# Performance work log

Hardware: AMD Instinct MI355X
Metric: run time of the kernel (lower is better)

## Reference

```python
import jax, jax.numpy as jnp
import numpy as np

D_MODEL = 1024
NUM_HEADS = 16
DEPTH = D_MODEL // NUM_HEADS


def setup_inputs() -> dict:
    key = jax.random.key(0)
    ks = jax.random.split(key, 11)
    B, S = 2, 2048
    s = 1.0 / np.sqrt(D_MODEL)
    inp = {
        'query': jax.random.normal(ks[0], (B, S, D_MODEL), jnp.float32),
        'key': jax.random.normal(ks[1], (B, S, D_MODEL), jnp.float32),
        'value': jax.random.normal(ks[2], (B, S, D_MODEL), jnp.float32),
        'Wq': jax.random.normal(ks[3], (D_MODEL, D_MODEL), jnp.float32) * s,
        'bq': jnp.zeros((D_MODEL,), jnp.float32),
        'Wk': jax.random.normal(ks[4], (D_MODEL, D_MODEL), jnp.float32) * s,
        'bk': jnp.zeros((D_MODEL,), jnp.float32),
        'Wv': jax.random.normal(ks[5], (D_MODEL, D_MODEL), jnp.float32) * s,
        'bv': jnp.zeros((D_MODEL,), jnp.float32),
        'Wo': jax.random.normal(ks[6], (D_MODEL, D_MODEL), jnp.float32) * s,
        'bo': jnp.zeros((D_MODEL,), jnp.float32),
    }
    return inp


def reference(query, key, value, Wq, bq, Wk, bk, Wv, bv, Wo, bo):
    B, S, _ = query.shape
    # QKV projections (nn.Linear: x @ W.T + b; here W stored as [in,out])
    Q = query @ Wq + bq
    K = key @ Wk + bk
    V = value @ Wv + bv
    # [B, H, S, depth]
    Q = Q.reshape(B, S, NUM_HEADS, DEPTH).transpose(0, 2, 1, 3)
    K = K.reshape(B, S, NUM_HEADS, DEPTH).transpose(0, 2, 1, 3)
    V = V.reshape(B, S, NUM_HEADS, DEPTH).transpose(0, 2, 1, 3)
    scores = jnp.einsum('bhqd,bhkd->bhqk', Q, K) / jnp.sqrt(jnp.float32(DEPTH))
    weights = jax.nn.softmax(scores, axis=-1)
    out = jnp.einsum('bhqk,bhkd->bhqd', weights, V)
    out = out.transpose(0, 2, 1, 3).reshape(B, S, D_MODEL)
    return out @ Wo + bo
```

## Files before the change

### kernel.cpp

```cpp
#include <hip/hip_runtime.h>
#include <stdint.h>

#define D_MODEL 1024
#define NHEAD   16
#define DEPTH   64
#define BATCH   2
#define SEQ     2048
#define M_ROWS  (BATCH*SEQ)

typedef __attribute__((ext_vector_type(8))) short short8;
typedef __attribute__((ext_vector_type(4))) float f32x4;
typedef _Float16 __attribute__((ext_vector_type(8))) half8;
typedef __fp16 __attribute__((ext_vector_type(2))) fp16x2;

__device__ __forceinline__ unsigned short f2b(float f) {
    union { float f; uint32_t u; } v; v.f = f;
    uint32_t r = (v.u + 0x7FFFu + ((v.u >> 16) & 1u)) >> 16;
    return (unsigned short)r;
}
__device__ __forceinline__ unsigned short f2h(float f) {
    union { _Float16 h; unsigned short u; } c; c.h = (_Float16)f; return c.u;
}
__device__ __forceinline__ unsigned int pkh(float a, float b) {
    union { fp16x2 h; unsigned int u; } c;
    c.h = __builtin_amdgcn_cvt_pkrtz(a, b);
    return c.u;
}
__device__ __forceinline__ float exp2fast(float x) {
#if defined(__has_builtin) && __has_builtin(__builtin_amdgcn_exp2f)
    return __builtin_amdgcn_exp2f(x);
#else
    return exp2f(x);
#endif
}

__device__ __forceinline__ void glds16(const void* g, void* l) {
    __builtin_amdgcn_global_load_lds(
        (const __attribute__((address_space(1))) unsigned int*)(uintptr_t)g,
        (__attribute__((address_space(3))) unsigned int*)(unsigned int)(uintptr_t)l,
        16, 0, 0);
}

__global__ __launch_bounds__(256) void prep(
    const float* __restrict__ q, const float* __restrict__ k, const float* __restrict__ v,
    unsigned short* __restrict__ xq, unsigned short* __restrict__ xk, unsigned short* __restrict__ xv,
    const float* __restrict__ w0, const float* __restrict__ w1,
    const float* __restrict__ w2, const float* __restrict__ w3,
    unsigned short* __restrict__ t0, unsigned short* __restrict__ t1,
    unsigned short* __restrict__ t2, unsigned short* __restrict__ t3)
{
    __shared__ unsigned short tile[64][65];
    const int bid = blockIdx.x, tid = threadIdx.x;
    if (bid < 12288) {
        const int t = bid >> 12;
        const float* s = (t == 0) ? q : (t == 1) ? k : v;
        unsigned short* d = (t == 0) ? xq : (t == 1) ? xk : xv;
        int i = (bid & 4095) * 256 + tid;
        float4 val = ((const float4*)s)[i];
        ushort4 u;
        u.x = f2b(val.x); u.y = f2b(val.y); u.z = f2b(val.z); u.w = f2b(val.w);
        ((ushort4*)d)[i] = u;
    } else {
        const int r3 = bid - 12288;
        const int z = r3 >> 8, by = (r3 & 255) >> 4, bx = r3 & 15;
        const float* w; unsigned short* t;
        switch (z) {
            case 0:  w = w0; t = t0; break;
            case 1:  w = w1; t = t1; break;
            case 2:  w = w2; t = t2; break;
            default: w = w3; t = t3; break;
        }
        const float sc = (z == 0) ? 0.125f * 1.44269504089f : 1.0f;
        const int k0 = by * 64, n0 = bx * 64;
        #pragma unroll
        for (int i = 0; i < 16; ++i) {
            int idx = i * 256 + tid;
            int r = idx >> 6, c = idx & 63;
            tile[c][r] = f2b(w[(size_t)(k0 + r) * D_MODEL + n0 + c] * sc);
        }
        __syncthreads();
        #pragma unroll
        for (int i = 0; i < 16; ++i) {
            int idx = i * 256 + tid;
            int r = idx >> 6, c = idx & 63;
            t[(size_t)(n0 + r) * D_MODEL + k0 + c] = tile[r][c];
        }
    }
}

template<int OUT_MODE, bool BIAS_M>
__device__ __forceinline__ void gemm_body(
    const unsigned short* __restrict__ A, const unsigned short* __restrict__ Bt,
    const float* __restrict__ bias, float bscale, void* __restrict__ Cv,
    int m0, int n0, int N, int K, unsigned short* As, unsigned short* Bs)
{
    const int tid  = threadIdx.x;
    const int lane = tid & 63;
    const int wave = tid >> 6;
    const int wm = wave & 1, wn = wave >> 1;
    const int quad = lane >> 4, l16 = lane & 15;

    auto stage = [&](int buf, int k0) {
        unsigned short* Ad = As + buf * (128 * 32);
        unsigned short* Bd = Bs + buf * (128 * 32);
        #pragma unroll
        for (int i = 0; i < 2; ++i) {
            int c = i * 256 + tid;
            int row = c >> 2, cb = c & 3;
            glds16(A  + (size_t)(m0 + row) * K + k0 + cb * 8, Ad + c * 8);
            glds16(Bt + (size_t)(n0 + row) * K + k0 + cb * 8, Bd + c * 8);
        }
    };

    f32x4 acc[4][4] = {};
    float bn[4];
    if (!BIAS_M) {
        #pragma unroll
        for (int nt = 0; nt < 4; ++nt) bn[nt] = bias[n0 + wn * 64 + nt * 16 + l16] * bscale;
    }

    stage(0, 0);
    const int NIT = K / 32;
    for (int it = 0; it < NIT; ++it) {
        __syncthreads();
        const unsigned short* Ab = As + (it & 1) * (128 * 32);
        const unsigned short* Bb = Bs + (it & 1) * (128 * 32);
        if (it + 1 < NIT) stage((it + 1) & 1, (it + 1) * 32);
        short8 af[4], bg[4];
        #pragma unroll
        for (int t = 0; t < 4; ++t) {
            af[t] = *(const short8*)&Ab[(wm * 64 + t * 16 + l16) * 32 + quad * 8];
            bg[t] = *(const short8*)&Bb[(wn * 64 + t * 16 + l16) * 32 + quad * 8];
        }
        #pragma unroll
        for (int mt = 0; mt < 4; ++mt)
            #pragma unroll
            for (int nt = 0; nt < 4; ++nt)
                acc[mt][nt] = __builtin_amdgcn_mfma_f32_16x16x32_bf16(af[mt], bg[nt], acc[mt][nt], 0, 0, 0);
    }

    #pragma unroll
    for (int mt = 0; mt < 4; ++mt)
        #pragma unroll
        for (int nt = 0; nt < 4; ++nt)
            #pragma unroll
            for (int r = 0; r < 4; ++r) {
                int m = m0 + wm * 64 + mt * 16 + quad * 4 + r;
                int n = n0 + wn * 64 + nt * 16 + l16;
                float bv_ = BIAS_M ? bias[m] * bscale : bn[nt];
                float val = acc[mt][nt][r] + bv_;
                if (OUT_MODE == 1)      ((unsigned short*)Cv)[(size_t)m * N + n] = f2b(val);
                else if (OUT_MODE == 2) ((unsigned short*)Cv)[(size_t)m * N + n] = f2h(val);
                else                    ((float*)Cv)[(size_t)m * N + n] = val;
            }
}

__global__ __launch_bounds__(256, 3) void gemm_qkvt(
    const unsigned short* __restrict__ xq, const unsigned short* __restrict__ xk,
    const unsigned short* __restrict__ xv, const unsigned short* __restrict__ wT,
    const float* __restrict__ bq, const float* __restrict__ bk, const float* __restrict__ bv,
    unsigned short* __restrict__ Qb, unsigned short* __restrict__ Kb, unsigned short* __restrict__ Vtg)
{
    __shared__ __align__(16) unsigned short As[2 * 128 * 32];
    __shared__ __align__(16) unsigned short Bs[2 * 128 * 32];
    const int z = blockIdx.y, t = blockIdx.x;
    const size_t wn = (size_t)D_MODEL * D_MODEL;
    if (z < 2) {
        int m0 = (t >> 3) * 128, n0 = (t & 7) * 128;
        gemm_body<1, false>(z ? xk : xq, wT + z * wn, z ? bk : bq, z ? 1.0f : 0.125f * 1.44269504089f,
                            z ? Kb : Qb, m0, n0, D_MODEL, D_MODEL, As, Bs);
    } else {
        int m0 = (t & 7) * 128, n0 = (t >> 3) * 128;
        gemm_body<2, true>(wT + 2 * wn, xv, bv, 1.0f, Vtg, m0, n0, M_ROWS, D_MODEL, As, Bs);
    }
}

__global__ __launch_bounds__(256, 2) void gemm_out(
    const unsigned short* __restrict__ A, const unsigned short* __restrict__ Bt,
    const float* __restrict__ bias, float* __restrict__ C)
{
    __shared__ __align__(16) unsigned short As[2 * 128 * 32];
    __shared__ __align__(16) unsigned short Bs[2 * 64 * 32];
    const int tid  = threadIdx.x;
    const int lane = tid & 63;
    const int wave = tid >> 6;
    const int wm = wave & 1, wn = wave >> 1;
    const int quad = lane >> 4, l16 = lane & 15;
    const int m0 = (blockIdx.x >> 4) * 128, n0 = (blockIdx.x & 15) * 64;
    const int N = D_MODEL, K = D_MODEL;

    auto stage = [&](int buf, int k0) {
        unsigned short* Ad = As + buf * (128 * 32);
        unsigned short* Bd = Bs + buf * (64 * 32);
        #pragma unroll
        for (int i = 0; i < 2; ++i) {
            int c = i * 256 + tid;
            int row = c >> 2, cb = c & 3;
            glds16(A + (size_t)(m0 + row) * K + k0 + cb * 8, Ad + c * 8);
        }
        int c = tid, row = c >> 2, cb = c & 3;
        glds16(Bt + (size_t)(n0 + row) * K + k0 + cb * 8, Bd + c * 8);
    };

    f32x4 acc[4][2] = {};
    float bn[2];
    #pragma unroll
    for (int nt = 0; nt < 2; ++nt) bn[nt] = bias[n0 + wn * 32 + nt * 16 + l16];

    stage(0, 0);
    const int NIT = K / 32;
    for (int it = 0; it < NIT; ++it) {
        __syncthreads();
        const unsigned short* Ab = As + (it & 1) * (128 * 32);
        const unsigned short* Bb = Bs + (it & 1) * (64 * 32);
        if (it + 1 < NIT) stage((it + 1) & 1, (it + 1) * 32);
        short8 af[4], bg[2];
        #pragma unroll
        for (int t = 0; t < 4; ++t)
            af[t] = *(const short8*)&Ab[(wm * 64 + t * 16 + l16) * 32 + quad * 8];
        #pragma unroll
        for (int t = 0; t < 2; ++t)
            bg[t] = *(const short8*)&Bb[(wn * 32 + t * 16 + l16) * 32 + quad * 8];
        #pragma unroll
        for (int mt = 0; mt < 4; ++mt)
            #pragma unroll
            for (int nt = 0; nt < 2; ++nt)
                acc[mt][nt] = __builtin_amdgcn_mfma_f32_16x16x32_bf16(af[mt], bg[nt], acc[mt][nt], 0, 0, 0);
    }

    #pragma unroll
    for (int mt = 0; mt < 4; ++mt)
        #pragma unroll
        for (int nt = 0; nt < 2; ++nt)
            #pragma unroll
            for (int r = 0; r < 4; ++r) {
                int m = m0 + wm * 64 + mt * 16 + quad * 4 + r;
                int n = n0 + wn * 32 + nt * 16 + l16;
                C[(size_t)m * N + n] = acc[mt][nt][r] + bn[nt];
            }
}

__global__ __launch_bounds__(256, 3) void attn_mfma(
    const unsigned short* __restrict__ Qb, const unsigned short* __restrict__ Kb,
    const unsigned short* __restrict__ Vtg, unsigned short* __restrict__ ctx)
{
    __shared__ __align__(16) unsigned short Ks[2][64 * 64];
    __shared__ __align__(16) unsigned short Vs[2][64 * 64];
    __shared__ __align__(16) unsigned short Ps[4][32 * 64];

    const int tid = threadIdx.x, lane = tid & 63, wave = tid >> 6;
    const int quad = lane >> 4, l16 = lane & 15;
    const int b = blockIdx.z, h = blockIdx.y;
    const int q0 = blockIdx.x * 128 + wave * 32;
    unsigned short* Psw = Ps[wave];

    short8 bqf[2][2];
    #pragma unroll
    for (int nt = 0; nt < 2; ++nt)
        #pragma unroll
        for (int ks = 0; ks < 2; ++ks)
            bqf[nt][ks] = *(const short8*)(Qb +
                (size_t)(b * SEQ + q0 + nt * 16 + l16) * D_MODEL + h * DEPTH + ks * 32 + quad * 8);

    const unsigned short* Kbase = Kb  + (size_t)b * SEQ * D_MODEL + h * DEPTH;
    const unsigned short* Vbase = Vtg + (size_t)h * DEPTH * M_ROWS + (size_t)b * SEQ;

    const int srow = lane >> 3;
    const int schunk = (lane & 7) ^ srow;
    auto stage = [&](int buf, int kt) {
        const unsigned short* Kt = Kbase + (size_t)kt * 64 * D_MODEL;
        const unsigned short* Vt = Vbase + kt * 64;
        #pragma unroll
        for (int i = 0; i < 2; ++i) {
            int g = i * 4 + wave;
            int row = g * 8 + srow;
            glds16(Kt + (size_t)row * D_MODEL + schunk * 8, &Ks[buf][g * 512 + lane * 8]);
            glds16(Vt + (size_t)row * M_ROWS  + schunk * 8, &Vs[buf][g * 512 + lane * 8]);
        }
    };

    const int x7 = l16 & 7;
    f32x4 o[2][4] = {};
    float lsum[2] = {0.f, 0.f};

    stage(0, 0);
    for (int kt = 0; kt < SEQ / 64; ++kt) {
        __syncthreads();
        const int buf = kt & 1;
        if (kt + 1 < SEQ / 64) stage(buf ^ 1, kt + 1);
        const unsigned short* Kf = Ks[buf];
        const unsigned short* Vf = Vs[buf];

        f32x4 s[4][2] = {};
        #pragma unroll
        for (int mt = 0; mt < 4; ++mt) {
            short8 ak[2];
            #pragma unroll
            for (int ks = 0; ks < 2; ++ks)
                ak[ks] = *(const short8*)&Kf[(mt * 16 + l16) * 64 + ((ks * 4 + quad) ^ x7) * 8];
            #pragma unroll
            for (int nt = 0; nt < 2; ++nt)
                #pragma unroll
                for (int ks = 0; ks < 2; ++ks)
                    s[mt][nt] = __builtin_amdgcn_mfma_f32_16x16x32_bf16(ak[ks], bqf[nt][ks], s[mt][nt], 0, 0, 0);
        }

        #pragma unroll
        for (int mt = 0; mt < 4; ++mt)
            #pragma unroll
            for (int nt = 0; nt < 2; ++nt) {
                float p0 = exp2fast(fminf(s[mt][nt][0], 14.4f));
                float p1 = exp2fast(fminf(s[mt][nt][1], 14.4f));
                float p2 = exp2fast(fminf(s[mt][nt][2], 14.4f));
                float p3 = exp2fast(fminf(s[mt][nt][3], 14.4f));
                lsum[nt] += (p0 + p1) + (p2 + p3);
                uint2 u; u.x = pkh(p0, p1); u.y = pkh(p2, p3);
                *(uint2*)&Psw[(nt * 16 + l16) * 64 +
                              (((mt * 2 + (quad >> 1)) ^ x7) * 8 + (quad & 1) * 4)] = u;
            }

        #pragma unroll
        for (int ks = 0; ks < 2; ++ks) {
            half8 ap[2], bvf[4];
            #pragma unroll
            for (int mq = 0; mq < 2; ++mq)
                ap[mq] = *(const half8*)&Psw[(mq * 16 + l16) * 64 + ((ks * 4 + quad) ^ x7) * 8];
            #pragma unroll
            for (int nd = 0; nd < 4; ++nd)
                bvf[nd] = *(const half8*)&Vf[(nd * 16 + l16) * 64 + ((ks * 4 + quad) ^ x7) * 8];
            #pragma unroll
            for (int mq = 0; mq < 2; ++mq)
                #pragma unroll
                for (int nd = 0; nd < 4; ++nd)
                    o[mq][nd] = __builtin_amdgcn_mfma_f32_16x16x32_f16(ap[mq], bvf[nd], o[mq][nd], 0, 0, 0);
        }
    }

    float linv[2];
    #pragma unroll
    for (int nt = 0; nt < 2; ++nt) {
        float t = lsum[nt];
        t += __shfl_xor(t, 16);
        t += __shfl_xor(t, 32);
        linv[nt] = 1.0f / t;
    }
    #pragma unroll
    for (int mq = 0; mq < 2; ++mq)
        #pragma unroll
        for (int r = 0; r < 4; ++r) {
            float li = __shfl(linv[mq], quad * 4 + r);
            #pragma unroll
            for (int nd = 0; nd < 4; ++nd)
                ctx[(size_t)(b * SEQ + q0 + mq * 16 + quad * 4 + r) * D_MODEL +
                    h * DEPTH + nd * 16 + l16] = f2b(o[mq][nd][r] * li);
        }
}

extern "C" void kernel_launch(void* const* d_in, const int* in_sizes, int n_in,
                              void* d_out, int out_size, void* d_ws, size_t ws_size,
                              hipStream_t stream)
{
    const float* query = (const float*)d_in[0];
    const float* key   = (const float*)d_in[1];
    const float* value = (const float*)d_in[2];
    const float* Wq = (const float*)d_in[3];
    const float* bq = (const float*)d_in[4];
    const float* Wk = (const float*)d_in[5];
    const float* bk = (const float*)d_in[6];
    const float* Wv = (const float*)d_in[7];
    const float* bv = (const float*)d_in[8];
    const float* Wo = (const float*)d_in[9];
    const float* bo = (const float*)d_in[10];

    char* ws = (char*)d_ws;
    size_t off = 0;
    auto alloc = [&](size_t bytes) -> char* {
        char* p = ws + off;
        off += (bytes + 255) & ~(size_t)255;
        return p;
    };
    const size_t xn = (size_t)M_ROWS * D_MODEL;
    const size_t wn = (size_t)D_MODEL * D_MODEL;
    unsigned short* xq   = (unsigned short*)alloc(xn * 2);
    unsigned short* xk   = (unsigned short*)alloc(xn * 2);
    unsigned short* xv   = (unsigned short*)alloc(xn * 2);
    unsigned short* wT   = (unsigned short*)alloc(3 * wn * 2);
    unsigned short* woT  = (unsigned short*)alloc(wn * 2);
    unsigned short* Qb   = (unsigned short*)alloc(xn * 2);
    unsigned short* Kb   = (unsigned short*)alloc(xn * 2);
    unsigned short* Vtg  = (unsigned short*)alloc(xn * 2);
    unsigned short* ctx  = (unsigned short*)alloc(xn * 2);
    if (off > ws_size) return;

    prep<<<dim3(13312), 256, 0, stream>>>(
        query, key, value, xq, xk, xv,
        Wq, Wk, Wv, Wo, wT, wT + wn, wT + 2 * wn, woT);
    gemm_qkvt<<<dim3(256, 3), 256, 0, stream>>>(xq, xk, xv, wT, bq, bk, bv, Qb, Kb, Vtg);
    attn_mfma<<<dim3(SEQ / 128, NHEAD, BATCH), 256, 0, stream>>>(Qb, Kb, Vtg, ctx);
    gemm_out<<<dim3(512), 256, 0, stream>>>(ctx, woT, bo, (float*)d_out);
}
```

Measured before the change: 225.7 us.

## Split attention over key halves with combine pass and shrink GEMM tiles

Attention now splits the key sequence into two halves, one per block. Each block writes unnormalized bf16 partial outputs and row sums to the workspace, and a new combine kernel adds the halves and normalizes them. This doubles the attention grid, which was meant to fill more CUs. The QKV and output GEMMs are moved onto a templated body with smaller 128x64 and 64x64 tiles and higher occupancy bounds, which gives more blocks. The cost is an extra kernel launch, extra global traffic for the partial outputs, and less data reuse per GEMM tile.

```diff
diff --git a/kernel.cpp b/kernel.cpp
--- a/kernel.cpp
+++ b/kernel.cpp
@@ -7,6 +7,8 @@
 #define BATCH   2
 #define SEQ     2048
 #define M_ROWS  (BATCH*SEQ)
+#define KTILES  (SEQ/64)
+#define KHALF   (KTILES/2)
 
 typedef __attribute__((ext_vector_type(8))) short short8;
 typedef __attribute__((ext_vector_type(4))) float f32x4;
@@ -20,6 +22,9 @@
 }
 __device__ __forceinline__ unsigned short f2h(float f) {
     union { _Float16 h; unsigned short u; } c; c.h = (_Float16)f; return c.u;
+}
+__device__ __forceinline__ float bits2f(unsigned int u) {
+    union { unsigned int u; float f; } c; c.u = u; return c.f;
 }
 __device__ __forceinline__ unsigned int pkh(float a, float b) {
     union { fp16x2 h; unsigned int u; } c;
@@ -33,7 +38,6 @@
     return exp2f(x);
 #endif
 }
-
 __device__ __forceinline__ void glds16(const void* g, void* l) {
     __builtin_amdgcn_global_load_lds(
         (const __attribute__((address_space(1))) unsigned int*)(uintptr_t)g,
@@ -88,12 +92,13 @@
     }
 }
 
-template<int OUT_MODE, bool BIAS_M>
+template<int MT, int NT, int OUT_MODE, bool BIAS_M>
 __device__ __forceinline__ void gemm_body(
     const unsigned short* __restrict__ A, const unsigned short* __restrict__ Bt,
     const float* __restrict__ bias, float bscale, void* __restrict__ Cv,
     int m0, int n0, int N, int K, unsigned short* As, unsigned short* Bs)
 {
+    constexpr int FM = MT / 32, FN = NT / 32;
     const int tid  = threadIdx.x;
     const int lane = tid & 63;
     const int wave = tid >> 6;
@@ -101,52 +106,56 @@
     const int quad = lane >> 4, l16 = lane & 15;
 
     auto stage = [&](int buf, int k0) {
-        unsigned short* Ad = As + buf * (128 * 32);
-        unsigned short* Bd = Bs + buf * (128 * 32);
-        #pragma unroll
-        for (int i = 0; i < 2; ++i) {
-            int c = i * 256 + tid;
-            int row = c >> 2, cb = c & 3;
-            glds16(A  + (size_t)(m0 + row) * K + k0 + cb * 8, Ad + c * 8);
+        unsigned short* Ad = As + buf * (MT * 32);
+        unsigned short* Bd = Bs + buf * (NT * 32);
+        #pragma unroll
+        for (int i = 0; i < MT / 64; ++i) {
+            int c = i * 256 + tid, row = c >> 2, cb = c & 3;
+            glds16(A + (size_t)(m0 + row) * K + k0 + cb * 8, Ad + c * 8);
+        }
+        #pragma unroll
+        for (int i = 0; i < NT / 64; ++i) {
+            int c = i * 256 + tid, row = c >> 2, cb = c & 3;
             glds16(Bt + (size_t)(n0 + row) * K + k0 + cb * 8, Bd + c * 8);
         }
     };
 
-    f32x4 acc[4][4] = {};
-    float bn[4];
+    f32x4 acc[FM][FN] = {};
+    float bn[FN];
     if (!BIAS_M) {
         #pragma unroll
-        for (int nt = 0; nt < 4; ++nt) bn[nt] = bias[n0 + wn * 64 + nt * 16 + l16] * bscale;
+        for (int nt = 0; nt < FN; ++nt) bn[nt] = bias[n0 + wn * (NT / 2) + nt * 16 + l16] * bscale;
     }
 
     stage(0, 0);
     const int NIT = K / 32;
     for (int it = 0; it < NIT; ++it) {
         __syncthreads();
-        const unsigned short* Ab = As + (it & 1) * (128 * 32);
-        const unsigned short* Bb = Bs + (it & 1) * (128 * 32);
+        const unsigned short* Ab = As + (it & 1) * (MT * 32);
+        const unsigned short* Bb = Bs + (it & 1) * (NT * 32);
         if (it + 1 < NIT) stage((it + 1) & 1, (it + 1) * 32);
-        short8 af[4], bg[4];
-        #pragma unroll
-        for (int t = 0; t < 4; ++t) {
-            af[t] = *(const short8*)&Ab[(wm * 64 + t * 16 + l16) * 32 + quad * 8];
-            bg[t] = *(const short8*)&Bb[(wn * 64 + t * 16 + l16) * 32 + quad * 8];
-        }
-        #pragma unroll
-        for (int mt = 0; mt < 4; ++mt)
-            #pragma unroll
-            for (int nt = 0; nt < 4; ++nt)
+        short8 af[FM], bg[FN];
+        #pragma unroll
+        for (int t = 0; t < FM; ++t)
+            af[t] = *(const short8*)&Ab[(wm * (MT / 2) + t * 16 + l16) * 32 + quad * 8];
+        #pragma unroll
+        for (int t = 0; t < FN; ++t)
+            bg[t] = *(const short8*)&Bb[(wn * (NT / 2) + t * 16 + l16) * 32 + quad * 8];
+        #pragma unroll
+        for (int mt = 0; mt < FM; ++mt)
+            #pragma unroll
+            for (int nt = 0; nt < FN; ++nt)
                 acc[mt][nt] = __builtin_amdgcn_mfma_f32_16x16x32_bf16(af[mt], bg[nt], acc[mt][nt], 0, 0, 0);
     }
 
     #pragma unroll
-    for (int mt = 0; mt < 4; ++mt)
-        #pragma unroll
-        for (int nt = 0; nt < 4; ++nt)
+    for (int mt = 0; mt < FM; ++mt)
+        #pragma unroll
+        for (int nt = 0; nt < FN; ++nt)
             #pragma unroll
             for (int r = 0; r < 4; ++r) {
-                int m = m0 + wm * 64 + mt * 16 + quad * 4 + r;
-                int n = n0 + wn * 64 + nt * 16 + l16;
+                int m = m0 + wm * (MT / 2) + mt * 16 + quad * 4 + r;
+                int n = n0 + wn * (NT / 2) + nt * 16 + l16;
                 float bv_ = BIAS_M ? bias[m] * bscale : bn[nt];
                 float val = acc[mt][nt][r] + bv_;
                 if (OUT_MODE == 1)      ((unsigned short*)Cv)[(size_t)m * N + n] = f2b(val);
@@ -155,94 +164,42 @@
             }
 }
 
-__global__ __launch_bounds__(256, 3) void gemm_qkvt(
+__global__ __launch_bounds__(256, 4) void gemm_qkvt(
     const unsigned short* __restrict__ xq, const unsigned short* __restrict__ xk,
     const unsigned short* __restrict__ xv, const unsigned short* __restrict__ wT,
     const float* __restrict__ bq, const float* __restrict__ bk, const float* __restrict__ bv,
     unsigned short* __restrict__ Qb, unsigned short* __restrict__ Kb, unsigned short* __restrict__ Vtg)
 {
     __shared__ __align__(16) unsigned short As[2 * 128 * 32];
-    __shared__ __align__(16) unsigned short Bs[2 * 128 * 32];
+    __shared__ __align__(16) unsigned short Bs[2 * 64 * 32];
     const int z = blockIdx.y, t = blockIdx.x;
     const size_t wn = (size_t)D_MODEL * D_MODEL;
     if (z < 2) {
-        int m0 = (t >> 3) * 128, n0 = (t & 7) * 128;
-        gemm_body<1, false>(z ? xk : xq, wT + z * wn, z ? bk : bq, z ? 1.0f : 0.125f * 1.44269504089f,
-                            z ? Kb : Qb, m0, n0, D_MODEL, D_MODEL, As, Bs);
+        int m0 = (t >> 4) * 128, n0 = (t & 15) * 64;
+        gemm_body<128, 64, 1, false>(z ? xk : xq, wT + z * wn, z ? bk : bq,
+                                     z ? 1.0f : 0.125f * 1.44269504089f,
+                                     z ? Kb : Qb, m0, n0, D_MODEL, D_MODEL, As, Bs);
     } else {
-        int m0 = (t & 7) * 128, n0 = (t >> 3) * 128;
-        gemm_body<2, true>(wT + 2 * wn, xv, bv, 1.0f, Vtg, m0, n0, M_ROWS, D_MODEL, As, Bs);
-    }
-}
-
-__global__ __launch_bounds__(256, 2) void gemm_out(
+        int m0 = (t & 7) * 128, n0 = (t >> 3) * 64;
+        gemm_body<128, 64, 2, true>(wT + 2 * wn, xv, bv, 1.0f, Vtg, m0, n0, M_ROWS, D_MODEL, As, Bs);
+    }
+}
+
+__global__ __launch_bounds__(256, 4) void gemm_out(
     const unsigned short* __restrict__ A, const unsigned short* __restrict__ Bt,
     const float* __restrict__ bias, float* __restrict__ C)
 {
-    __shared__ __align__(16) unsigned short As[2 * 128 * 32];
+    __shared__ __align__(16) unsigned short As[2 * 64 * 32];
     __shared__ __align__(16) unsigned short Bs[2 * 64 * 32];
-    const int tid  = threadIdx.x;
-    const int lane = tid & 63;
-    const int wave = tid >> 6;
-    const int wm = wave & 1, wn = wave >> 1;
-    const int quad = lane >> 4, l16 = lane & 15;
-    const int m0 = (blockIdx.x >> 4) * 128, n0 = (blockIdx.x & 15) * 64;
-    const int N = D_MODEL, K = D_MODEL;
-
-    auto stage = [&](int buf, int k0) {
-        unsigned short* Ad = As + buf * (128 * 32);
-        unsigned short* Bd = Bs + buf * (64 * 32);
-        #pragma unroll
-        for (int i = 0; i < 2; ++i) {
-            int c = i * 256 + tid;
-            int row = c >> 2, cb = c & 3;
-            glds16(A + (size_t)(m0 + row) * K + k0 + cb * 8, Ad + c * 8);
-        }
-        int c = tid, row = c >> 2, cb = c & 3;
-        glds16(Bt + (size_t)(n0 + row) * K + k0 + cb * 8, Bd + c * 8);
-    };
-
-    f32x4 acc[4][2] = {};
-    float bn[2];
-    #pragma unroll
-    for (int nt = 0; nt < 2; ++nt) bn[nt] = bias[n0 + wn * 32 + nt * 16 + l16];
-
-    stage(0, 0);
-    const int NIT = K / 32;
-    for (int it = 0; it < NIT; ++it) {
-        __syncthreads();
-        const unsigned short* Ab = As + (it & 1) * (128 * 32);
-        const unsigned short* Bb = Bs + (it & 1) * (64 * 32);
-        if (it + 1 < NIT) stage((it + 1) & 1, (it + 1) * 32);
-        short8 af[4], bg[2];
-        #pragma unroll
-        for (int t = 0; t < 4; ++t)
-            af[t] = *(const short8*)&Ab[(wm * 64 + t * 16 + l16) * 32 + quad * 8];
-        #pragma unroll
-        for (int t = 0; t < 2; ++t)
-            bg[t] = *(const short8*)&Bb[(wn * 32 + t * 16 + l16) * 32 + quad * 8];
-        #pragma unroll
-        for (int mt = 0; mt < 4; ++mt)
-            #pragma unroll
-            for (int nt = 0; nt < 2; ++nt)
-                acc[mt][nt] = __builtin_amdgcn_mfma_f32_16x16x32_bf16(af[mt], bg[nt], acc[mt][nt], 0, 0, 0);
-    }
-
-    #pragma unroll
-    for (int mt = 0; mt < 4; ++mt)
-        #pragma unroll
-        for (int nt = 0; nt < 2; ++nt)
-            #pragma unroll
-            for (int r = 0; r < 4; ++r) {
-                int m = m0 + wm * 64 + mt * 16 + quad * 4 + r;
-                int n = n0 + wn * 32 + nt * 16 + l16;
-                C[(size_t)m * N + n] = acc[mt][nt][r] + bn[nt];
-            }
+    const int t = blockIdx.x;
+    gemm_body<64, 64, 0, false>(A, Bt, bias, 1.0f, C,
+                                (t >> 4) * 64, (t & 15) * 64, D_MODEL, D_MODEL, As, Bs);
 }
 
 __global__ __launch_bounds__(256, 3) void attn_mfma(
     const unsigned short* __restrict__ Qb, const unsigned short* __restrict__ Kb,
-    const unsigned short* __restrict__ Vtg, unsigned short* __restrict__ ctx)
+    const unsigned short* __restrict__ Vtg,
+    unsigned short* __restrict__ Oh, float* __restrict__ L)
 {
     __shared__ __align__(16) unsigned short Ks[2][64 * 64];
     __shared__ __align__(16) unsigned short Vs[2][64 * 64];
@@ -251,7 +208,8 @@
     const int tid = threadIdx.x, lane = tid & 63, wave = tid >> 6;
     const int quad = lane >> 4, l16 = lane & 15;
     const int b = blockIdx.z, h = blockIdx.y;
-    const int q0 = blockIdx.x * 128 + wave * 32;
+    const int qt = blockIdx.x >> 1, kh = blockIdx.x & 1;
+    const int q0 = qt * 128 + wave * 32;
     unsigned short* Psw = Ps[wave];
 
     short8 bqf[2][2];
@@ -283,11 +241,11 @@
     f32x4 o[2][4] = {};
     float lsum[2] = {0.f, 0.f};
 
-    stage(0, 0);
-    for (int kt = 0; kt < SEQ / 64; ++kt) {
+    stage(0, kh * KHALF);
+    for (int k2 = 0; k2 < KHALF; ++k2) {
         __syncthreads();
-        const int buf = kt & 1;
-        if (kt + 1 < SEQ / 64) stage(buf ^ 1, kt + 1);
+        const int buf = k2 & 1;
+        if (k2 + 1 < KHALF) stage(buf ^ 1, kh * KHALF + k2 + 1);
         const unsigned short* Kf = Ks[buf];
         const unsigned short* Vf = Vs[buf];
 
@@ -336,24 +294,54 @@
         }
     }
 
-    float linv[2];
+    unsigned short* Oq = Oh + (size_t)kh * M_ROWS * D_MODEL;
+    #pragma unroll
+    for (int mq = 0; mq < 2; ++mq)
+        #pragma unroll
+        for (int r = 0; r < 4; ++r) {
+            int row = b * SEQ + q0 + mq * 16 + quad * 4 + r;
+            #pragma unroll
+            for (int nd = 0; nd < 4; ++nd)
+                Oq[(size_t)row * D_MODEL + h * DEPTH + nd * 16 + l16] = f2b(o[mq][nd][r]);
+        }
+    float lred[2];
     #pragma unroll
     for (int nt = 0; nt < 2; ++nt) {
         float t = lsum[nt];
         t += __shfl_xor(t, 16);
         t += __shfl_xor(t, 32);
-        linv[nt] = 1.0f / t;
-    }
-    #pragma unroll
-    for (int mq = 0; mq < 2; ++mq)
-        #pragma unroll
-        for (int r = 0; r < 4; ++r) {
-            float li = __shfl(linv[mq], quad * 4 + r);
-            #pragma unroll
-            for (int nd = 0; nd < 4; ++nd)
-                ctx[(size_t)(b * SEQ + q0 + mq * 16 + quad * 4 + r) * D_MODEL +
-                    h * DEPTH + nd * 16 + l16] = f2b(o[mq][nd][r] * li);
-        }
+        lred[nt] = t;
+    }
+    if (quad == 0) {
+        #pragma unroll
+        for (int nt = 0; nt < 2; ++nt)
+            L[(size_t)kh * M_ROWS * NHEAD +
+              (size_t)(b * SEQ + q0 + nt * 16 + l16) * NHEAD + h] = lred[nt];
+    }
+}
+
+__global__ __launch_bounds__(256) void combine(
+    const unsigned short* __restrict__ Oh, const float* __restrict__ L,
+    unsigned short* __restrict__ ctx)
+{
+    int i = blockIdx.x * 256 + threadIdx.x;
+    int flat8 = i * 8;
+    int row = flat8 >> 10;
+    int h = (flat8 & 1023) >> 6;
+    float inv = 1.0f / (L[(size_t)row * NHEAD + h] +
+                        L[(size_t)M_ROWS * NHEAD + (size_t)row * NHEAD + h]);
+    uint4 a = ((const uint4*)Oh)[i];
+    uint4 c4 = ((const uint4*)(Oh + (size_t)M_ROWS * D_MODEL))[i];
+    const unsigned int* ap = (const unsigned int*)&a;
+    const unsigned int* bp = (const unsigned int*)&c4;
+    unsigned int r[4];
+    #pragma unroll
+    for (int j = 0; j < 4; ++j) {
+        float lo = bits2f(ap[j] << 16) + bits2f(bp[j] << 16);
+        float hi = bits2f(ap[j] & 0xFFFF0000u) + bits2f(bp[j] & 0xFFFF0000u);
+        r[j] = (unsigned int)f2b(lo * inv) | ((unsigned int)f2b(hi * inv) << 16);
+    }
+    ((uint4*)ctx)[i] = *(uint4*)r;
 }
 
 extern "C" void kernel_launch(void* const* d_in, const int* in_sizes, int n_in,
@@ -389,13 +377,16 @@
     unsigned short* Qb   = (unsigned short*)alloc(xn * 2);
     unsigned short* Kb   = (unsigned short*)alloc(xn * 2);
     unsigned short* Vtg  = (unsigned short*)alloc(xn * 2);
+    unsigned short* Oh   = (unsigned short*)alloc(2 * xn * 2);
+    float*          L    = (float*)alloc(2 * (size_t)M_ROWS * NHEAD * 4);
     unsigned short* ctx  = (unsigned short*)alloc(xn * 2);
     if (off > ws_size) return;
 
     prep<<<dim3(13312), 256, 0, stream>>>(
         query, key, value, xq, xk, xv,
         Wq, Wk, Wv, Wo, wT, wT + wn, wT + 2 * wn, woT);
-    gemm_qkvt<<<dim3(256, 3), 256, 0, stream>>>(xq, xk, xv, wT, bq, bk, bv, Qb, Kb, Vtg);
-    attn_mfma<<<dim3(SEQ / 128, NHEAD, BATCH), 256, 0, stream>>>(Qb, Kb, Vtg, ctx);
-    gemm_out<<<dim3(512), 256, 0, stream>>>(ctx, woT, bo, (float*)d_out);
-}
+    gemm_qkvt<<<dim3(512, 3), 256, 0, stream>>>(xq, xk, xv, wT, bq, bk, bv, Qb, Kb, Vtg);
+    attn_mfma<<<dim3(32, NHEAD, BATCH), 256, 0, stream>>>(Qb, Kb, Vtg, Oh, L);
+    combine<<<dim3(2048), 256, 0, stream>>>(Oh, L, ctx);
+    gemm_out<<<dim3(1024), 256, 0, stream>>>(ctx, woT, bo, (float*)d_out);
+}
```

After: 238.4 us. +5.6%, slower.
